# Optimization experiments

Measured on AMD Instinct MI355X. Metric: run time of the kernel, lower is better.

## Reference

```python
import jax, jax.numpy as jnp
import numpy as np

B, L = 8192, 2048

def setup_inputs() -> dict:
    key = jax.random.key(0)
    k1, k2 = jax.random.split(key)
    x = jax.random.normal(k1, (B, L), dtype=jnp.float32)
    y = jax.random.normal(k2, (B, L), dtype=jnp.float32)
    # MRS ppm axis is descending; GABA/Glx windows lie inside [1, 5] ppm
    ppm = jnp.linspace(5.0, 1.0, L, dtype=jnp.float32)
    return {"x": x, "ppm": ppm, "y": y}

def _bounds(ppm_np, lo, hi):
    # matches torch: start = amin(where(ppm <= hi)), stop = amax(where(ppm >= lo))
    mn = int(np.min(np.where(ppm_np <= hi)[0]))
    mx = int(np.max(np.where(ppm_np >= lo)[0]))
    return mn, mx

def _norm01(v):
    vmin = v.min(axis=-1, keepdims=True)
    vmax = v.max(axis=-1, keepdims=True)
    return (v - vmin) / (vmax - vmin)

def _pearson(a, b):
    # row-wise Pearson correlation == corrcoef(cat([a,b]))[0,1], batched over rows
    am = a - a.mean(axis=-1, keepdims=True)
    bm = b - b.mean(axis=-1, keepdims=True)
    return (am * bm).sum(-1) / jnp.sqrt((am * am).sum(-1) * (bm * bm).sum(-1))

def _loss(x, y, ppm_np):
    # ---- ShapeScoreLoss (gaba 2.8-3.2, glx 3.6-3.9, weights 0.6/0.4) ----
    g_lo, g_hi = _bounds(ppm_np, 2.8, 3.2)
    gaba_score = _pearson(_norm01(x[:, g_lo:g_hi]), _norm01(y[:, g_lo:g_hi]))
    s_lo, s_hi = _bounds(ppm_np, 3.6, 3.9)
    glx_score = _pearson(_norm01(x[:, s_lo:s_hi]), _norm01(y[:, s_lo:s_hi]))
    shape_loss = 1.0 - (0.6 * gaba_score + 0.4 * glx_score).mean()
    # ---- RangeMAELoss (gaba 2.8-3.2, glx 3.55-3.95, weights 6/3/1 over 10) ----
    r_lo, r_hi = _bounds(ppm_np, 3.55, 3.95)
    gaba_mae = jnp.abs(x[:, g_lo:g_hi] - y[:, g_lo:g_hi]).mean()
    glx_mae = jnp.abs(x[:, r_lo:r_hi] - y[:, r_lo:r_hi]).mean()
    global_mae = jnp.abs(x - y).mean()
    range_loss = (gaba_mae * 6.0 + glx_mae * 3.0 + global_mae) / 10.0
    return shape_loss + range_loss * 0.5

def reference(x, ppm, y):
    ppm_np = np.asarray(ppm)  # ppm is a fixed axis -> static slice bounds
    return _loss(x, y, ppm_np)
```

## Files before the change

kernel.cpp:

```cpp
#include <hip/hip_runtime.h>

#define L_COLS 2048

typedef float vf4 __attribute__((ext_vector_type(4)));

__device__ __forceinline__ float wave_red(float v) {
#pragma unroll
    for (int m = 32; m >= 1; m >>= 1) v += __shfl_xor(v, m, 64);
    return v;
}

__global__ __launch_bounds__(64) void init_kernel(const float* __restrict__ ppm,
                                                  float* __restrict__ acc,
                                                  int* __restrict__ ob) {
    const int lane = threadIdx.x;
    if (lane < 4) acc[lane] = 0.f;

    int mn0 = 0x7fffffff, mn1 = 0x7fffffff, mn2 = 0x7fffffff;
    int mx0 = -1, mx1 = -1, mx2 = -1;
    const vf4* __restrict__ p4 = (const vf4*)ppm;
#pragma unroll
    for (int k = 0; k < L_COLS / 256; ++k) {
        const int j = k * 64 + lane;
        const vf4 pv = p4[j];
        const float ps[4] = {pv.x, pv.y, pv.z, pv.w};
#pragma unroll
        for (int e = 0; e < 4; ++e) {
            const int c = 4 * j + e;
            const float p = ps[e];
            if (p <= 3.2f)  mn0 = min(mn0, c);
            if (p >= 2.8f)  mx0 = max(mx0, c);
            if (p <= 3.9f)  mn1 = min(mn1, c);
            if (p >= 3.6f)  mx1 = max(mx1, c);
            if (p <= 3.95f) mn2 = min(mn2, c);
            if (p >= 3.55f) mx2 = max(mx2, c);
        }
    }
#pragma unroll
    for (int m = 32; m >= 1; m >>= 1) {
        mn0 = min(mn0, __shfl_xor(mn0, m, 64));
        mx0 = max(mx0, __shfl_xor(mx0, m, 64));
        mn1 = min(mn1, __shfl_xor(mn1, m, 64));
        mx1 = max(mx1, __shfl_xor(mx1, m, 64));
        mn2 = min(mn2, __shfl_xor(mn2, m, 64));
        mx2 = max(mx2, __shfl_xor(mx2, m, 64));
    }
    if (lane == 0) {
        ob[0] = mn0; ob[1] = mx0;
        ob[2] = mn1; ob[3] = mx1;
        ob[4] = mn2; ob[5] = mx2;
    }
}

__global__ __launch_bounds__(256, 2) void loss_main(const float* __restrict__ x,
                                                    const float* __restrict__ y,
                                                    const int* __restrict__ ob,
                                                    float* __restrict__ acc) {
    const int lane = threadIdx.x & 63;
    const int wv   = threadIdx.x >> 6;
    const long row = (long)blockIdx.x * 4 + wv;

    const int g_lo = ob[0], g_hi = ob[1];
    const int s_lo = ob[2], s_hi = ob[3];
    const int r_lo = ob[4], r_hi = ob[5];
    const int lo_any = min(min(g_lo, s_lo), r_lo);
    const int hi_any = max(max(g_hi, s_hi), r_hi);

    const vf4* __restrict__ x4 = (const vf4*)(x + row * L_COLS);
    const vf4* __restrict__ y4 = (const vf4*)(y + row * L_COLS);

    vf4 xr[8], yr[8];
#pragma unroll
    for (int k = 0; k < 8; ++k) {
        xr[k] = x4[k * 64 + lane];
        yr[k] = y4[k * 64 + lane];
    }
    __builtin_amdgcn_sched_barrier(0);

    float gl = 0.f;
    float a_sx = 0, a_sy = 0, a_xy = 0, a_xx = 0, a_yy = 0, a_mae = 0;
    float b_sx = 0, b_sy = 0, b_xy = 0, b_xx = 0, b_yy = 0;
    float r_mae = 0;

#pragma unroll
    for (int k = 0; k < 8; ++k) {
        const vf4 xv = xr[k];
        const vf4 yv = yr[k];
        const float d0 = fabsf(xv.x - yv.x), d1 = fabsf(xv.y - yv.y);
        const float d2 = fabsf(xv.z - yv.z), d3 = fabsf(xv.w - yv.w);
        gl += (d0 + d1) + (d2 + d3);

        if (k * 256 < hi_any && k * 256 + 256 > lo_any) {
            const float xs[4] = {xv.x, xv.y, xv.z, xv.w};
            const float ys[4] = {yv.x, yv.y, yv.z, yv.w};
            const float ds[4] = {d0, d1, d2, d3};
#pragma unroll
            for (int e = 0; e < 4; ++e) {
                const int c = k * 256 + 4 * lane + e;
                const float xe = xs[e], ye = ys[e];
                if (c >= g_lo && c < g_hi) {
                    a_sx += xe; a_sy += ye; a_xy += xe * ye;
                    a_xx += xe * xe; a_yy += ye * ye; a_mae += ds[e];
                }
                if (c >= s_lo && c < s_hi) {
                    b_sx += xe; b_sy += ye; b_xy += xe * ye;
                    b_xx += xe * xe; b_yy += ye * ye;
                }
                if (c >= r_lo && c < r_hi) r_mae += ds[e];
            }
        }
    }

    gl    = wave_red(gl);
    a_sx  = wave_red(a_sx);  a_sy = wave_red(a_sy);
    a_xy  = wave_red(a_xy);  a_xx = wave_red(a_xx);  a_yy = wave_red(a_yy);
    a_mae = wave_red(a_mae);
    b_sx  = wave_red(b_sx);  b_sy = wave_red(b_sy);
    b_xy  = wave_red(b_xy);  b_xx = wave_red(b_xx);  b_yy = wave_red(b_yy);
    r_mae = wave_red(r_mae);

    __shared__ float part[4][4];
    if (lane == 0) {
        const float ng = (float)(g_hi - g_lo);
        const float ns = (float)(s_hi - s_lo);
        const float covA = a_xy - a_sx * a_sy / ng;
        const float vAx  = a_xx - a_sx * a_sx / ng;
        const float vAy  = a_yy - a_sy * a_sy / ng;
        const float scoreA = covA * rsqrtf(vAx * vAy);
        const float covB = b_xy - b_sx * b_sy / ns;
        const float vBx  = b_xx - b_sx * b_sx / ns;
        const float vBy  = b_yy - b_sy * b_sy / ns;
        const float scoreB = covB * rsqrtf(vBx * vBy);
        part[wv][0] = 0.6f * scoreA + 0.4f * scoreB;
        part[wv][1] = a_mae;
        part[wv][2] = r_mae;
        part[wv][3] = gl;
    }
    __syncthreads();
    if (threadIdx.x < 4) {
        const float s = part[0][threadIdx.x] + part[1][threadIdx.x] +
                        part[2][threadIdx.x] + part[3][threadIdx.x];
        atomicAdd(&acc[threadIdx.x], s);
    }
}

__global__ void finalize_kernel(const float* __restrict__ acc, const int* __restrict__ ob,
                                int Brows, float* __restrict__ out) {
    const float ng = (float)(ob[1] - ob[0]);
    const float nr = (float)(ob[5] - ob[4]);
    const float Bf = (float)Brows;
    const float shape_loss = 1.f - acc[0] / Bf;
    const float gaba_mae = acc[1] / (Bf * ng);
    const float glx_mae  = acc[2] / (Bf * nr);
    const float glob_mae = acc[3] / (Bf * (float)L_COLS);
    const float range_loss = (gaba_mae * 6.f + glx_mae * 3.f + glob_mae) * 0.1f;
    out[0] = shape_loss + range_loss * 0.5f;
}

extern "C" void kernel_launch(void* const* d_in, const int* in_sizes, int n_in,
                              void* d_out, int out_size, void* d_ws, size_t ws_size,
                              hipStream_t stream) {
    const float* x   = (const float*)d_in[0];
    const float* ppm = (const float*)d_in[1];
    const float* y   = (const float*)d_in[2];
    const int L = in_sizes[1];
    const int Brows = in_sizes[0] / L;

    float* acc = (float*)d_ws;
    int*   ob  = (int*)((char*)d_ws + 64);

    init_kernel<<<1, 64, 0, stream>>>(ppm, acc, ob);
    loss_main<<<Brows / 4, 256, 0, stream>>>(x, y, ob, acc);
    finalize_kernel<<<1, 1, 0, stream>>>(acc, ob, Brows, (float*)d_out);
}
```

Measured before the change: 46.44 us.

## Stage rows via global_load_lds and spread atomics over 64 accumulator slots

Loads each row of x and y straight into LDS with the global_load_lds intrinsic instead of into registers, then reads them back from LDS for the reductions. The per-block shared-memory combine and __syncthreads are dropped: each wave atomically adds its partials into one of 64 slots picked by row, and a 64-lane finalize kernel sums the slots. The goal is to cut register pressure and atomic contention on a single address. In exchange, each block now needs 64KB of LDS, which limits occupancy, adds an LDS round trip, and quadruples the number of atomics.

```diff
diff --git a/kernel.cpp b/kernel.cpp
--- a/kernel.cpp
+++ b/kernel.cpp
@@ -1,6 +1,7 @@
 #include <hip/hip_runtime.h>
 
 #define L_COLS 2048
+#define NSLOT 64
 
 typedef float vf4 __attribute__((ext_vector_type(4)));
 
@@ -10,11 +11,17 @@
     return v;
 }
 
+__device__ __forceinline__ void gload_lds16(const float* g, float* l) {
+    __builtin_amdgcn_global_load_lds((const __attribute__((address_space(1))) void*)g,
+                                     (__attribute__((address_space(3))) void*)l,
+                                     16, 0, 0);
+}
+
 __global__ __launch_bounds__(64) void init_kernel(const float* __restrict__ ppm,
                                                   float* __restrict__ acc,
                                                   int* __restrict__ ob) {
     const int lane = threadIdx.x;
-    if (lane < 4) acc[lane] = 0.f;
+    ((vf4*)acc)[lane] = (vf4){0.f, 0.f, 0.f, 0.f};
 
     int mn0 = 0x7fffffff, mn1 = 0x7fffffff, mn2 = 0x7fffffff;
     int mx0 = -1, mx1 = -1, mx2 = -1;
@@ -52,10 +59,11 @@
     }
 }
 
-__global__ __launch_bounds__(256, 2) void loss_main(const float* __restrict__ x,
-                                                    const float* __restrict__ y,
-                                                    const int* __restrict__ ob,
-                                                    float* __restrict__ acc) {
+__global__ __launch_bounds__(256) void loss_main(const float* __restrict__ x,
+                                                 const float* __restrict__ y,
+                                                 const int* __restrict__ ob,
+                                                 float* __restrict__ acc) {
+    __shared__ float smem[4 * 4096];
     const int lane = threadIdx.x & 63;
     const int wv   = threadIdx.x >> 6;
     const long row = (long)blockIdx.x * 4 + wv;
@@ -66,16 +74,17 @@
     const int lo_any = min(min(g_lo, s_lo), r_lo);
     const int hi_any = max(max(g_hi, s_hi), r_hi);
 
-    const vf4* __restrict__ x4 = (const vf4*)(x + row * L_COLS);
-    const vf4* __restrict__ y4 = (const vf4*)(y + row * L_COLS);
+    const float* __restrict__ xr = x + row * L_COLS;
+    const float* __restrict__ yr = y + row * L_COLS;
+    float* const wx = smem + wv * 4096;
+    float* const wy = wx + 2048;
 
-    vf4 xr[8], yr[8];
 #pragma unroll
     for (int k = 0; k < 8; ++k) {
-        xr[k] = x4[k * 64 + lane];
-        yr[k] = y4[k * 64 + lane];
+        gload_lds16(xr + k * 256 + lane * 4, wx + k * 256);
+        gload_lds16(yr + k * 256 + lane * 4, wy + k * 256);
     }
-    __builtin_amdgcn_sched_barrier(0);
+    asm volatile("s_waitcnt vmcnt(0)" ::: "memory");
 
     float gl = 0.f;
     float a_sx = 0, a_sy = 0, a_xy = 0, a_xx = 0, a_yy = 0, a_mae = 0;
@@ -84,8 +93,8 @@
 
 #pragma unroll
     for (int k = 0; k < 8; ++k) {
-        const vf4 xv = xr[k];
-        const vf4 yv = yr[k];
+        const vf4 xv = ((const vf4*)(wx + k * 256))[lane];
+        const vf4 yv = ((const vf4*)(wy + k * 256))[lane];
         const float d0 = fabsf(xv.x - yv.x), d1 = fabsf(xv.y - yv.y);
         const float d2 = fabsf(xv.z - yv.z), d3 = fabsf(xv.w - yv.w);
         gl += (d0 + d1) + (d2 + d3);
@@ -119,7 +128,6 @@
     b_xy  = wave_red(b_xy);  b_xx = wave_red(b_xx);  b_yy = wave_red(b_yy);
     r_mae = wave_red(r_mae);
 
-    __shared__ float part[4][4];
     if (lane == 0) {
         const float ng = (float)(g_hi - g_lo);
         const float ns = (float)(s_hi - s_lo);
@@ -131,30 +139,34 @@
         const float vBx  = b_xx - b_sx * b_sx / ns;
         const float vBy  = b_yy - b_sy * b_sy / ns;
         const float scoreB = covB * rsqrtf(vBx * vBy);
-        part[wv][0] = 0.6f * scoreA + 0.4f * scoreB;
-        part[wv][1] = a_mae;
-        part[wv][2] = r_mae;
-        part[wv][3] = gl;
-    }
-    __syncthreads();
-    if (threadIdx.x < 4) {
-        const float s = part[0][threadIdx.x] + part[1][threadIdx.x] +
-                        part[2][threadIdx.x] + part[3][threadIdx.x];
-        atomicAdd(&acc[threadIdx.x], s);
+        float* slot = acc + 4 * ((int)row & (NSLOT - 1));
+        atomicAdd(&slot[0], 0.6f * scoreA + 0.4f * scoreB);
+        atomicAdd(&slot[1], a_mae);
+        atomicAdd(&slot[2], r_mae);
+        atomicAdd(&slot[3], gl);
     }
 }
 
-__global__ void finalize_kernel(const float* __restrict__ acc, const int* __restrict__ ob,
-                                int Brows, float* __restrict__ out) {
-    const float ng = (float)(ob[1] - ob[0]);
-    const float nr = (float)(ob[5] - ob[4]);
-    const float Bf = (float)Brows;
-    const float shape_loss = 1.f - acc[0] / Bf;
-    const float gaba_mae = acc[1] / (Bf * ng);
-    const float glx_mae  = acc[2] / (Bf * nr);
-    const float glob_mae = acc[3] / (Bf * (float)L_COLS);
-    const float range_loss = (gaba_mae * 6.f + glx_mae * 3.f + glob_mae) * 0.1f;
-    out[0] = shape_loss + range_loss * 0.5f;
+__global__ __launch_bounds__(64) void finalize_kernel(const float* __restrict__ acc,
+                                                      const int* __restrict__ ob,
+                                                      int Brows, float* __restrict__ out) {
+    const int lane = threadIdx.x;
+    vf4 v = ((const vf4*)acc)[lane];
+    v.x = wave_red(v.x);
+    v.y = wave_red(v.y);
+    v.z = wave_red(v.z);
+    v.w = wave_red(v.w);
+    if (lane == 0) {
+        const float ng = (float)(ob[1] - ob[0]);
+        const float nr = (float)(ob[5] - ob[4]);
+        const float Bf = (float)Brows;
+        const float shape_loss = 1.f - v.x / Bf;
+        const float gaba_mae = v.y / (Bf * ng);
+        const float glx_mae  = v.z / (Bf * nr);
+        const float glob_mae = v.w / (Bf * (float)L_COLS);
+        const float range_loss = (gaba_mae * 6.f + glx_mae * 3.f + glob_mae) * 0.1f;
+        out[0] = shape_loss + range_loss * 0.5f;
+    }
 }
 
 extern "C" void kernel_launch(void* const* d_in, const int* in_sizes, int n_in,
@@ -167,9 +179,9 @@
     const int Brows = in_sizes[0] / L;
 
     float* acc = (float*)d_ws;
-    int*   ob  = (int*)((char*)d_ws + 64);
+    int*   ob  = (int*)((char*)d_ws + 1024);
 
     init_kernel<<<1, 64, 0, stream>>>(ppm, acc, ob);
     loss_main<<<Brows / 4, 256, 0, stream>>>(x, y, ob, acc);
-    finalize_kernel<<<1, 1, 0, stream>>>(acc, ob, Brows, (float*)d_out);
+    finalize_kernel<<<1, 64, 0, stream>>>(acc, ob, Brows, (float*)d_out);
 }
```

New measurement: 82.54 us. 1.78x slower.
